# Optimization experiments

Hardware: AMD Instinct MI355X
Metric: run time of the kernel (lower is better)

The kernel has to match this reference:

```python
import jax, jax.numpy as jnp
import numpy as np

B, T, D = 8, 1024, 1024
H, G = 16, 4            # num_heads, query_groups
HD = D // H             # head_dim = 64
REP = H // G            # heads_per_group
EPS = 1e-10
NEG = -1e9


def setup_inputs() -> dict:
    key = jax.random.key(0)
    k1, k2, k3 = jax.random.split(key, 3)
    x = jax.random.normal(k1, (B, T, D), dtype=jnp.float32)
    w_qkv = jax.random.normal(k2, (D, H * HD + 2 * G * HD), dtype=jnp.float32) * (D ** -0.5)
    w_o = jax.random.normal(k3, (D, D), dtype=jnp.float32) * (D ** -0.5)
    padding_mask = jnp.ones((B, T), dtype=bool)
    return {"x": x, "w_qkv": w_qkv, "w_o": w_o, "padding_mask": padding_mask}


def _l2_norm(t):
    # qk_norm_type=2: L2 normalize over head_dim
    return t / (jnp.sqrt(jnp.sum(t * t, axis=-1, keepdims=True)) + EPS)


def reference(x, w_qkv, w_o, padding_mask):
    # fused QKV projection: [B,T,D] @ [D, H*HD + 2*G*HD]
    qkv = x @ w_qkv
    q, k, v = jnp.split(qkv, [H * HD, H * HD + G * HD], axis=-1)
    q = q.reshape(B, T, H, HD)
    k = k.reshape(B, T, G, HD)
    v = v.reshape(B, T, G, HD)
    # QK normalization (L2 over head_dim)
    q = _l2_norm(q)
    k = _l2_norm(k)
    # GQA: expand KV heads (repeat_interleave along head dim)
    k = jnp.repeat(k, REP, axis=2)  # [B,T,H,HD]
    v = jnp.repeat(v, REP, axis=2)
    # to [B,H,T,HD]
    q = q.transpose(0, 2, 1, 3)
    k = k.transpose(0, 2, 1, 3)
    v = v.transpose(0, 2, 1, 3)
    # causal + padding mask, True = attend
    causal = jnp.tril(jnp.ones((T, T), dtype=bool))  # [T_q, T_k]
    valid = padding_mask[:, None, :, None] & padding_mask[:, None, None, :] & causal[None, None]
    scale = HD ** -0.5  # SDPA default scale
    scores = jnp.einsum('bhqd,bhkd->bhqk', q, k) * scale
    scores = jnp.where(valid, scores, NEG)
    attn = jax.nn.softmax(scores, axis=-1)
    out = jnp.einsum('bhqk,bhkd->bhqd', attn, v)  # [B,H,T,HD]
    out = out.transpose(0, 2, 1, 3).reshape(B, T, D)
    return out @ w_o
```

## Files before the change

### kernel.cpp

```cpp
#include <hip/hip_runtime.h>
#include <hip/hip_bf16.h>

typedef __attribute__((ext_vector_type(8))) short short8;
typedef __attribute__((ext_vector_type(4))) short short4v;
typedef __attribute__((ext_vector_type(4))) float f32x4;

#define B_ 8
#define T_ 1024
#define D_ 1024
#define H_ 16
#define G_ 4
#define HD_ 64
#define QKVW 1536

#define GLOAD16(gp, lp) __builtin_amdgcn_global_load_lds( \
    (const __attribute__((address_space(1))) void*)(gp),  \
    (__attribute__((address_space(3))) void*)(lp), 16, 0, 0)

__device__ __forceinline__ float exp2_fast(float x) {
    return __builtin_amdgcn_exp2f(x);
}

__device__ __forceinline__ short8 pack_bf16x8(float4 a, float4 b) {
    union { short8 s; __hip_bfloat16 h[8]; } u;
    u.h[0] = __float2bfloat16(a.x); u.h[1] = __float2bfloat16(a.y);
    u.h[2] = __float2bfloat16(a.z); u.h[3] = __float2bfloat16(a.w);
    u.h[4] = __float2bfloat16(b.x); u.h[5] = __float2bfloat16(b.y);
    u.h[6] = __float2bfloat16(b.z); u.h[7] = __float2bfloat16(b.w);
    return u.s;
}

__global__ __launch_bounds__(256) void cvt_transpose(
    const float* __restrict__ in, __hip_bfloat16* __restrict__ outT, int K, int N)
{
    __shared__ float tile[32][33];
    const int k0 = blockIdx.y * 32, n0 = blockIdx.x * 32;
    const int r = threadIdx.x >> 5, c = threadIdx.x & 31;
    #pragma unroll
    for (int i = 0; i < 4; ++i)
        tile[r + i * 8][c] = in[(size_t)(k0 + r + i * 8) * N + n0 + c];
    __syncthreads();
    #pragma unroll
    for (int i = 0; i < 4; ++i)
        outT[(size_t)(n0 + r + i * 8) * K + k0 + c] = __float2bfloat16(tile[c][r + i * 8]);
}

__global__ __launch_bounds__(256) void gemm_qkv(
    const float* __restrict__ Af,
    const __hip_bfloat16* __restrict__ Bt,
    __hip_bfloat16* __restrict__ qkv,
    __hip_bfloat16* __restrict__ vt)
{
    const int M = B_ * T_, K = D_;
    __shared__ __hip_bfloat16 As[2][128 * 32];
    __shared__ __hip_bfloat16 Bs[2][128 * 32];

    const int tid  = threadIdx.x;
    const int lane = tid & 63;
    const int wr   = (tid >> 6) >> 1;
    const int wc   = (tid >> 6) & 1;

    const int rpx = (M >> 7) >> 3;
    const int xcd = blockIdx.x & 7;
    const int lin = blockIdx.x >> 3;
    const int by  = xcd * rpx + (lin % rpx);
    const int bx  = lin / rpx;
    const int m0 = by * 128;
    const int n0 = bx * 128;

    f32x4 acc[4][4] = {};

    const int sr0 = tid >> 2;
    const int sr1 = 64 + sr0;
    const int slot  = (tid & 3) ^ ((tid >> 3) & 3);
    const int sc_ln = (tid & 3) * 8;
    const int sc_sw = slot * 8;
    const int ws0 = sr0 * 64 + slot * 16;
    const int ws1 = sr1 * 64 + slot * 16;

    const float* Ar0f = Af + (size_t)(m0 + sr0) * K + sc_ln;
    const float* Ar1f = Af + (size_t)(m0 + sr1) * K + sc_ln;
    const __hip_bfloat16* Br0 = Bt + (size_t)(n0 + sr0) * K + sc_sw;
    const __hip_bfloat16* Br1 = Bt + (size_t)(n0 + sr1) * K + sc_sw;

    const int fr = lane & 15;
    const int kb = (lane >> 4) * 16;
    const int swzg = ((fr >> 1) & 3) << 4;

    float4 a0a = *(const float4*)(Ar0f);
    float4 a0b = *(const float4*)(Ar0f + 4);
    float4 a1a = *(const float4*)(Ar1f);
    float4 a1b = *(const float4*)(Ar1f + 4);
    GLOAD16(Br0, (char*)&Bs[0][0] + tid * 16);
    GLOAD16(Br1, (char*)&Bs[0][0] + 4096 + tid * 16);
    *(short8*)((char*)&As[0][0] + ws0) = pack_bf16x8(a0a, a0b);
    *(short8*)((char*)&As[0][0] + ws1) = pack_bf16x8(a1a, a1b);
    __syncthreads();

    int cur = 0;
    for (int kk = 0; kk < K; kk += 32) {
        const int nxt = cur ^ 1;
        const bool more = (kk + 32 < K);
        if (more) {
            a0a = *(const float4*)(Ar0f + kk + 32);
            a0b = *(const float4*)(Ar0f + kk + 36);
            a1a = *(const float4*)(Ar1f + kk + 32);
            a1b = *(const float4*)(Ar1f + kk + 36);
            GLOAD16(Br0 + kk + 32, (char*)&Bs[nxt][0] + tid * 16);
            GLOAD16(Br1 + kk + 32, (char*)&Bs[nxt][0] + 4096 + tid * 16);
        }
        short8 a[4], b[4];
        #pragma unroll
        for (int m = 0; m < 4; ++m)
            a[m] = *(const short8*)((char*)&As[cur][0] +
                    (wr * 64 + m * 16 + fr) * 64 + (kb ^ swzg));
        #pragma unroll
        for (int n = 0; n < 4; ++n)
            b[n] = *(const short8*)((char*)&Bs[cur][0] +
                    (wc * 64 + n * 16 + fr) * 64 + (kb ^ swzg));
        #pragma unroll
        for (int m = 0; m < 4; ++m)
            #pragma unroll
            for (int n = 0; n < 4; ++n)
                acc[m][n] = __builtin_amdgcn_mfma_f32_16x16x32_bf16(a[m], b[n], acc[m][n], 0, 0, 0);
        if (more) {
            *(short8*)((char*)&As[nxt][0] + ws0) = pack_bf16x8(a0a, a0b);
            *(short8*)((char*)&As[nxt][0] + ws1) = pack_bf16x8(a1a, a1b);
        }
        __syncthreads();
        cur = nxt;
    }

    const int rowb  = m0 + wr * 64 + (lane >> 4) * 4;
    const int colb0 = n0 + wc * 64;

    if (n0 < 1280) {
        const float extra = (n0 < 1024) ? 0.18033688f : 1.0f;
        #pragma unroll
        for (int m = 0; m < 4; ++m)
            #pragma unroll
            for (int r = 0; r < 4; ++r) {
                float ss = 0.f;
                #pragma unroll
                for (int n = 0; n < 4; ++n) { float v = acc[m][n][r]; ss += v * v; }
                ss += __shfl_xor(ss, 1, 64);
                ss += __shfl_xor(ss, 2, 64);
                ss += __shfl_xor(ss, 4, 64);
                ss += __shfl_xor(ss, 8, 64);
                float sc = extra / (sqrtf(ss) + 1e-10f);
                const size_t rbase = (size_t)(rowb + m * 16 + r) * QKVW + colb0 + fr;
                #pragma unroll
                for (int n = 0; n < 4; ++n)
                    qkv[rbase + n * 16] = __float2bfloat16(acc[m][n][r] * sc);
            }
    } else {
        #pragma unroll
        for (int m = 0; m < 4; ++m) {
            const int row = rowb + m * 16;
            const int bb  = row >> 10;
            const int t0  = row & 1023;
            #pragma unroll
            for (int n = 0; n < 4; ++n) {
                const int cv = colb0 + fr + n * 16 - 1280;
                const int gg = cv >> 6, d = cv & 63;
                union { short4v s; __hip_bfloat16 h[4]; } u;
                u.h[0] = __float2bfloat16(acc[m][n][0]);
                u.h[1] = __float2bfloat16(acc[m][n][1]);
                u.h[2] = __float2bfloat16(acc[m][n][2]);
                u.h[3] = __float2bfloat16(acc[m][n][3]);
                *reinterpret_cast<short4v*>(
                    vt + ((size_t)((bb * G_ + gg) * HD_ + d)) * T_ + t0) = u.s;
            }
        }
    }
}

__global__ __launch_bounds__(256) void gemm_tn_f32(
    const __hip_bfloat16* __restrict__ A,
    const __hip_bfloat16* __restrict__ Bt,
    float* __restrict__ C, int M, int N, int K)
{
    __shared__ __hip_bfloat16 As[2][128 * 32];
    __shared__ __hip_bfloat16 Bs[2][128 * 32];

    const int tid  = threadIdx.x;
    const int lane = tid & 63;
    const int wr   = (tid >> 6) >> 1;
    const int wc   = (tid >> 6) & 1;

    const int rpx = (M >> 7) >> 3;
    const int xcd = blockIdx.x & 7;
    const int lin = blockIdx.x >> 3;
    const int by  = xcd * rpx + (lin % rpx);
    const int bx  = lin / rpx;
    const int m0 = by * 128;
    const int n0 = bx * 128;

    f32x4 acc[4][4] = {};

    const int sr0 = tid >> 2;
    const int sr1 = 64 + sr0;
    const int slot  = (tid & 3) ^ ((tid >> 3) & 3);
    const int sc_sw = slot * 8;

    const __hip_bfloat16* Ar0 = A  + (size_t)(m0 + sr0) * K + sc_sw;
    const __hip_bfloat16* Ar1 = A  + (size_t)(m0 + sr1) * K + sc_sw;
    const __hip_bfloat16* Br0 = Bt + (size_t)(n0 + sr0) * K + sc_sw;
    const __hip_bfloat16* Br1 = Bt + (size_t)(n0 + sr1) * K + sc_sw;

    const int fr = lane & 15;
    const int kb = (lane >> 4) * 16;
    const int swzg = ((fr >> 1) & 3) << 4;

    GLOAD16(Ar0, (char*)&As[0][0] + tid * 16);
    GLOAD16(Ar1, (char*)&As[0][0] + 4096 + tid * 16);
    GLOAD16(Br0, (char*)&Bs[0][0] + tid * 16);
    GLOAD16(Br1, (char*)&Bs[0][0] + 4096 + tid * 16);
    __syncthreads();

    int cur = 0;
    for (int kk = 0; kk < K; kk += 32) {
        const int nxt = cur ^ 1;
        if (kk + 32 < K) {
            GLOAD16(Ar0 + kk + 32, (char*)&As[nxt][0] + tid * 16);
            GLOAD16(Ar1 + kk + 32, (char*)&As[nxt][0] + 4096 + tid * 16);
            GLOAD16(Br0 + kk + 32, (char*)&Bs[nxt][0] + tid * 16);
            GLOAD16(Br1 + kk + 32, (char*)&Bs[nxt][0] + 4096 + tid * 16);
        }
        short8 a[4], b[4];
        #pragma unroll
        for (int m = 0; m < 4; ++m)
            a[m] = *(const short8*)((char*)&As[cur][0] +
                    (wr * 64 + m * 16 + fr) * 64 + (kb ^ swzg));
        #pragma unroll
        for (int n = 0; n < 4; ++n)
            b[n] = *(const short8*)((char*)&Bs[cur][0] +
                    (wc * 64 + n * 16 + fr) * 64 + (kb ^ swzg));
        #pragma unroll
        for (int m = 0; m < 4; ++m)
            #pragma unroll
            for (int n = 0; n < 4; ++n)
                acc[m][n] = __builtin_amdgcn_mfma_f32_16x16x32_bf16(a[m], b[n], acc[m][n], 0, 0, 0);
        __syncthreads();
        cur = nxt;
    }

    const int rowb = m0 + wr * 64 + (lane >> 4) * 4;
    const int colb = n0 + wc * 64 + fr;
    #pragma unroll
    for (int m = 0; m < 4; ++m)
        #pragma unroll
        for (int n = 0; n < 4; ++n)
            #pragma unroll
            for (int r = 0; r < 4; ++r)
                C[(size_t)(rowb + m * 16 + r) * N + colb + n * 16] = acc[m][n][r];
}

__global__ __launch_bounds__(256) void attn_fwd(
    const __hip_bfloat16* __restrict__ qkv,
    const __hip_bfloat16* __restrict__ vt,
    __hip_bfloat16* __restrict__ out)
{
    const int pair = blockIdx.x;
    const int h  = blockIdx.y;
    const int b  = blockIdx.z;
    const int g  = h >> 2;

    const int tid  = threadIdx.x;
    const int lane = tid & 63;
    const int wid  = tid >> 6;

    __shared__ __hip_bfloat16 Ks[2 * 4096];
    __shared__ __hip_bfloat16 Vs[2 * 4096];
    __shared__ __hip_bfloat16 Ps[4 * 1024];

    const int fr  = lane & 15;
    const int kf  = (lane >> 4) * 8;
    const int kb  = kf * 2;
    const int swz = (fr & 7) << 4;

    const int srow = tid >> 3;
    const int scol = ((tid & 7) * 8) ^ ((srow & 7) << 3);

    const size_t kgbase = (size_t)(b * T_) * QKVW + H_ * HD_ + g * HD_ + scol;
    const size_t vgbase = (size_t)((b * G_ + g) * HD_) * T_ + scol;

    char* PsB = (char*)Ps + wid * 2048;

    auto stage = [&](int kt, int sl) {
        GLOAD16(qkv + kgbase + (size_t)(kt * 64 + srow) * QKVW,
                (char*)Ks + sl * 8192 + tid * 16);
        GLOAD16(qkv + kgbase + (size_t)(kt * 64 + 32 + srow) * QKVW,
                (char*)Ks + sl * 8192 + 4096 + tid * 16);
        GLOAD16(vt + vgbase + (size_t)srow * T_ + kt * 64,
                (char*)Vs + sl * 8192 + tid * 16);
        GLOAD16(vt + vgbase + (size_t)(32 + srow) * T_ + kt * 64,
                (char*)Vs + sl * 8192 + 4096 + tid * 16);
    };

    for (int half = 0; half < 2; ++half) {
        const int qt = half ? (15 - pair) : pair;
        const int q0 = qt * 64;
        const int arow  = q0 + wid * 16 + fr;
        const int rbase = q0 + wid * 16 + (lane >> 4) * 4;

        short8 qfrag0, qfrag1;
        {
            const size_t qbase = ((size_t)(b * T_ + arow)) * QKVW + h * HD_;
            qfrag0 = *(const short8*)(qkv + qbase + kf);
            qfrag1 = *(const short8*)(qkv + qbase + 32 + kf);
        }

        float lsum[4] = {0.f, 0.f, 0.f, 0.f};
        f32x4 o[4] = {};

        auto compute = [&](int kt, int sl, bool diag) {
            char* KsB = (char*)Ks + sl * 8192;
            char* VsB = (char*)Vs + sl * 8192;

            f32x4 s[4] = {};
            __builtin_amdgcn_s_setprio(1);
            #pragma unroll
            for (int nf = 0; nf < 4; ++nf) {
                const int row = fr + 16 * nf;
                short8 b0 = *(const short8*)(KsB + row * 128 + (kb ^ swz));
                short8 b1 = *(const short8*)(KsB + row * 128 + ((64 + kb) ^ swz));
                s[nf] = __builtin_amdgcn_mfma_f32_16x16x32_bf16(qfrag0, b0, s[nf], 0, 0, 0);
                s[nf] = __builtin_amdgcn_mfma_f32_16x16x32_bf16(qfrag1, b1, s[nf], 0, 0, 0);
            }
            __builtin_amdgcn_s_setprio(0);

            if (diag) {
                #pragma unroll
                for (int nf = 0; nf < 4; ++nf) {
                    int col = kt * 64 + fr + 16 * nf;
                    #pragma unroll
                    for (int r = 0; r < 4; ++r) {
                        float p = (col <= rbase + r) ? exp2_fast(s[nf][r]) : 0.f;
                        lsum[r] += p;
                        int q = (lane >> 4) * 4 + r;
                        *(__hip_bfloat16*)(PsB + q * 128 +
                            ((2 * (fr + 16 * nf)) ^ ((q & 7) << 4))) = __float2bfloat16(p);
                    }
                }
            } else {
                #pragma unroll
                for (int nf = 0; nf < 4; ++nf)
                    #pragma unroll
                    for (int r = 0; r < 4; ++r) {
                        float p = exp2_fast(s[nf][r]);
                        lsum[r] += p;
                        int q = (lane >> 4) * 4 + r;
                        *(__hip_bfloat16*)(PsB + q * 128 +
                            ((2 * (fr + 16 * nf)) ^ ((q & 7) << 4))) = __float2bfloat16(p);
                    }
            }

            short8 pa0 = *(const short8*)(PsB + fr * 128 + (kb ^ swz));
            short8 pa1 = *(const short8*)(PsB + fr * 128 + ((64 + kb) ^ swz));
            __builtin_amdgcn_s_setprio(1);
            #pragma unroll
            for (int nf = 0; nf < 4; ++nf) {
                const int row = fr + 16 * nf;
                short8 b0 = *(const short8*)(VsB + row * 128 + (kb ^ swz));
                short8 b1 = *(const short8*)(VsB + row * 128 + ((64 + kb) ^ swz));
                o[nf] = __builtin_amdgcn_mfma_f32_16x16x32_bf16(pa0, b0, o[nf], 0, 0, 0);
                o[nf] = __builtin_amdgcn_mfma_f32_16x16x32_bf16(pa1, b1, o[nf], 0, 0, 0);
            }
            __builtin_amdgcn_s_setprio(0);
        };

        int kt = 0;
        while (kt + 1 < qt) {
            stage(kt, 0);
            stage(kt + 1, 1);
            __syncthreads();
            compute(kt, 0, false);
            compute(kt + 1, 1, false);
            __syncthreads();
            kt += 2;
        }
        if (kt < qt) {
            stage(kt, 0);
            __syncthreads();
            compute(kt, 0, false);
            __syncthreads();
            kt += 1;
        }
        stage(qt, 0);
        __syncthreads();
        compute(qt, 0, true);
        __syncthreads();

        float linv[4];
        #pragma unroll
        for (int r = 0; r < 4; ++r) {
            float v = lsum[r];
            v += __shfl_xor(v, 1, 64);
            v += __shfl_xor(v, 2, 64);
            v += __shfl_xor(v, 4, 64);
            v += __shfl_xor(v, 8, 64);
            linv[r] = 1.0f / v;
        }
        #pragma unroll
        for (int nf = 0; nf < 4; ++nf) {
            int col = fr + 16 * nf;
            #pragma unroll
            for (int r = 0; r < 4; ++r) {
                float v = o[nf][r] * linv[r];
                out[((size_t)(b * T_ + rbase + r)) * (H_ * HD_) + h * HD_ + col] =
                    __float2bfloat16(v);
            }
        }
    }
}

extern "C" void kernel_launch(void* const* d_in, const int* in_sizes, int n_in,
                              void* d_out, int out_size, void* d_ws, size_t ws_size,
                              hipStream_t stream) {
    const float* x_f     = (const float*)d_in[0];
    const float* w_qkv_f = (const float*)d_in[1];
    const float* w_o_f   = (const float*)d_in[2];
    float* out = (float*)d_out;

    const int NX  = B_ * T_ * D_;
    const int NWQ = D_ * QKVW;
    const int NWO = D_ * D_;

    __hip_bfloat16* attn_out = (__hip_bfloat16*)d_ws;
    __hip_bfloat16* wqkvT = attn_out + NX;
    __hip_bfloat16* woT   = wqkvT + NWQ;
    __hip_bfloat16* qkv   = woT + NWO;
    __hip_bfloat16* vt    = qkv + (size_t)(B_ * T_) * QKVW;

    dim3 blk(256);

    cvt_transpose<<<dim3(QKVW / 32, D_ / 32), blk, 0, stream>>>(w_qkv_f, wqkvT, D_, QKVW);
    cvt_transpose<<<dim3(D_ / 32, D_ / 32), blk, 0, stream>>>(w_o_f, woT, D_, D_);

    gemm_qkv<<<dim3((QKVW / 128) * ((B_ * T_) / 128)), blk, 0, stream>>>(
        x_f, wqkvT, qkv, vt);

    attn_fwd<<<dim3(8, H_, B_), blk, 0, stream>>>(qkv, vt, attn_out);

    gemm_tn_f32<<<dim3((D_ / 128) * ((B_ * T_) / 128)), blk, 0, stream>>>(
        attn_out, woT, out, B_ * T_, D_, D_);
}
```

Before: 118.1 us.

## Enlarge attention query tile to 128 rows, two M-fragments per wave

The attention kernel now processes 128 query rows per block instead of 64, with each wave handling two 16-row fragments that share the K and V fragments loaded from LDS. This halves the number of blocks and the global K/V staging per query row, and reuses each LDS read of K/V for twice the MFMA work. It costs more registers and P scratch space and launches fewer blocks (512), which may hurt occupancy and load balance; the causal mask now covers the last two key tiles.

```diff
diff --git a/kernel.cpp b/kernel.cpp
--- a/kernel.cpp
+++ b/kernel.cpp
@@ -272,7 +272,7 @@
 
     __shared__ __hip_bfloat16 Ks[2 * 4096];
     __shared__ __hip_bfloat16 Vs[2 * 4096];
-    __shared__ __hip_bfloat16 Ps[4 * 1024];
+    __shared__ __hip_bfloat16 Ps[4 * 2048];
 
     const int fr  = lane & 15;
     const int kf  = (lane >> 4) * 8;
@@ -285,7 +285,7 @@
     const size_t kgbase = (size_t)(b * T_) * QKVW + H_ * HD_ + g * HD_ + scol;
     const size_t vgbase = (size_t)((b * G_ + g) * HD_) * T_ + scol;
 
-    char* PsB = (char*)Ps + wid * 2048;
+    char* PsB = (char*)Ps + wid * 4096;
 
     auto stage = [&](int kt, int sl) {
         GLOAD16(qkv + kgbase + (size_t)(kt * 64 + srow) * QKVW,
@@ -299,117 +299,125 @@
     };
 
     for (int half = 0; half < 2; ++half) {
-        const int qt = half ? (15 - pair) : pair;
-        const int q0 = qt * 64;
-        const int arow  = q0 + wid * 16 + fr;
-        const int rbase = q0 + wid * 16 + (lane >> 4) * 4;
-
-        short8 qfrag0, qfrag1;
-        {
-            const size_t qbase = ((size_t)(b * T_ + arow)) * QKVW + h * HD_;
-            qfrag0 = *(const short8*)(qkv + qbase + kf);
-            qfrag1 = *(const short8*)(qkv + qbase + 32 + kf);
-        }
-
-        float lsum[4] = {0.f, 0.f, 0.f, 0.f};
-        f32x4 o[4] = {};
-
-        auto compute = [&](int kt, int sl, bool diag) {
-            char* KsB = (char*)Ks + sl * 8192;
-            char* VsB = (char*)Vs + sl * 8192;
-
-            f32x4 s[4] = {};
-            __builtin_amdgcn_s_setprio(1);
-            #pragma unroll
-            for (int nf = 0; nf < 4; ++nf) {
-                const int row = fr + 16 * nf;
-                short8 b0 = *(const short8*)(KsB + row * 128 + (kb ^ swz));
-                short8 b1 = *(const short8*)(KsB + row * 128 + ((64 + kb) ^ swz));
-                s[nf] = __builtin_amdgcn_mfma_f32_16x16x32_bf16(qfrag0, b0, s[nf], 0, 0, 0);
-                s[nf] = __builtin_amdgcn_mfma_f32_16x16x32_bf16(qfrag1, b1, s[nf], 0, 0, 0);
-            }
-            __builtin_amdgcn_s_setprio(0);
-
-            if (diag) {
-                #pragma unroll
-                for (int nf = 0; nf < 4; ++nf) {
-                    int col = kt * 64 + fr + 16 * nf;
-                    #pragma unroll
-                    for (int r = 0; r < 4; ++r) {
-                        float p = (col <= rbase + r) ? exp2_fast(s[nf][r]) : 0.f;
-                        lsum[r] += p;
-                        int q = (lane >> 4) * 4 + r;
-                        *(__hip_bfloat16*)(PsB + q * 128 +
-                            ((2 * (fr + 16 * nf)) ^ ((q & 7) << 4))) = __float2bfloat16(p);
-                    }
-                }
-            } else {
-                #pragma unroll
-                for (int nf = 0; nf < 4; ++nf)
-                    #pragma unroll
-                    for (int r = 0; r < 4; ++r) {
-                        float p = exp2_fast(s[nf][r]);
-                        lsum[r] += p;
-                        int q = (lane >> 4) * 4 + r;
-                        *(__hip_bfloat16*)(PsB + q * 128 +
-                            ((2 * (fr + 16 * nf)) ^ ((q & 7) << 4))) = __float2bfloat16(p);
-                    }
-            }
-
-            short8 pa0 = *(const short8*)(PsB + fr * 128 + (kb ^ swz));
-            short8 pa1 = *(const short8*)(PsB + fr * 128 + ((64 + kb) ^ swz));
-            __builtin_amdgcn_s_setprio(1);
-            #pragma unroll
-            for (int nf = 0; nf < 4; ++nf) {
-                const int row = fr + 16 * nf;
-                short8 b0 = *(const short8*)(VsB + row * 128 + (kb ^ swz));
-                short8 b1 = *(const short8*)(VsB + row * 128 + ((64 + kb) ^ swz));
-                o[nf] = __builtin_amdgcn_mfma_f32_16x16x32_bf16(pa0, b0, o[nf], 0, 0, 0);
-                o[nf] = __builtin_amdgcn_mfma_f32_16x16x32_bf16(pa1, b1, o[nf], 0, 0, 0);
-            }
-            __builtin_amdgcn_s_setprio(0);
-        };
-
-        int kt = 0;
-        while (kt + 1 < qt) {
+        const int qt  = half ? (7 - pair) : pair;
+        const int q0  = qt * 128;
+        const int nkt = 2 * qt + 2;
+
+        short8 qf[2][2];
+        #pragma unroll
+        for (int m = 0; m < 2; ++m) {
+            const size_t qbase =
+                ((size_t)(b * T_ + q0 + wid * 32 + m * 16 + fr)) * QKVW + h * HD_;
+            qf[m][0] = *(const short8*)(qkv + qbase + kf);
+            qf[m][1] = *(const short8*)(qkv + qbase + 32 + kf);
+        }
+        const int rb0 = q0 + wid * 32 + (lane >> 4) * 4;
+
+        float lsum[2][4] = {};
+        f32x4 o[2][4] = {};
+
+        for (int kt = 0; kt < nkt; kt += 2) {
             stage(kt, 0);
             stage(kt + 1, 1);
             __syncthreads();
-            compute(kt, 0, false);
-            compute(kt + 1, 1, false);
+
+            #pragma unroll
+            for (int sl = 0; sl < 2; ++sl) {
+                const int  ck  = kt + sl;
+                const bool msk = (ck >= nkt - 2);
+                char* KsB = (char*)Ks + sl * 8192;
+                char* VsB = (char*)Vs + sl * 8192;
+
+                short8 bk0[4], bk1[4];
+                #pragma unroll
+                for (int nf = 0; nf < 4; ++nf) {
+                    const int row = fr + 16 * nf;
+                    bk0[nf] = *(const short8*)(KsB + row * 128 + (kb ^ swz));
+                    bk1[nf] = *(const short8*)(KsB + row * 128 + ((64 + kb) ^ swz));
+                }
+
+                #pragma unroll
+                for (int m = 0; m < 2; ++m) {
+                    f32x4 s[4] = {};
+                    __builtin_amdgcn_s_setprio(1);
+                    #pragma unroll
+                    for (int nf = 0; nf < 4; ++nf) {
+                        s[nf] = __builtin_amdgcn_mfma_f32_16x16x32_bf16(qf[m][0], bk0[nf], s[nf], 0, 0, 0);
+                        s[nf] = __builtin_amdgcn_mfma_f32_16x16x32_bf16(qf[m][1], bk1[nf], s[nf], 0, 0, 0);
+                    }
+                    __builtin_amdgcn_s_setprio(0);
+
+                    if (msk) {
+                        #pragma unroll
+                        for (int nf = 0; nf < 4; ++nf) {
+                            int col = ck * 64 + fr + 16 * nf;
+                            #pragma unroll
+                            for (int r = 0; r < 4; ++r) {
+                                float p = (col <= rb0 + m * 16 + r) ? exp2_fast(s[nf][r]) : 0.f;
+                                lsum[m][r] += p;
+                                int q = m * 16 + (lane >> 4) * 4 + r;
+                                *(__hip_bfloat16*)(PsB + q * 128 +
+                                    ((2 * (fr + 16 * nf)) ^ ((q & 7) << 4))) = __float2bfloat16(p);
+                            }
+                        }
+                    } else {
+                        #pragma unroll
+                        for (int nf = 0; nf < 4; ++nf)
+                            #pragma unroll
+                            for (int r = 0; r < 4; ++r) {
+                                float p = exp2_fast(s[nf][r]);
+                                lsum[m][r] += p;
+                                int q = m * 16 + (lane >> 4) * 4 + r;
+                                *(__hip_bfloat16*)(PsB + q * 128 +
+                                    ((2 * (fr + 16 * nf)) ^ ((q & 7) << 4))) = __float2bfloat16(p);
+                            }
+                    }
+                }
+
+                short8 bv0[4], bv1[4];
+                #pragma unroll
+                for (int nf = 0; nf < 4; ++nf) {
+                    const int row = fr + 16 * nf;
+                    bv0[nf] = *(const short8*)(VsB + row * 128 + (kb ^ swz));
+                    bv1[nf] = *(const short8*)(VsB + row * 128 + ((64 + kb) ^ swz));
+                }
+                __builtin_amdgcn_s_setprio(1);
+                #pragma unroll
+                for (int m = 0; m < 2; ++m) {
+                    short8 pa0 = *(const short8*)(PsB + (m * 16 + fr) * 128 + (kb ^ swz));
+                    short8 pa1 = *(const short8*)(PsB + (m * 16 + fr) * 128 + ((64 + kb) ^ swz));
+                    #pragma unroll
+                    for (int nf = 0; nf < 4; ++nf) {
+                        o[m][nf] = __builtin_amdgcn_mfma_f32_16x16x32_bf16(pa0, bv0[nf], o[m][nf], 0, 0, 0);
+                        o[m][nf] = __builtin_amdgcn_mfma_f32_16x16x32_bf16(pa1, bv1[nf], o[m][nf], 0, 0, 0);
+                    }
+                }
+                __builtin_amdgcn_s_setprio(0);
+            }
             __syncthreads();
-            kt += 2;
-        }
-        if (kt < qt) {
-            stage(kt, 0);
-            __syncthreads();
-            compute(kt, 0, false);
-            __syncthreads();
-            kt += 1;
-        }
-        stage(qt, 0);
-        __syncthreads();
-        compute(qt, 0, true);
-        __syncthreads();
-
-        float linv[4];
-        #pragma unroll
-        for (int r = 0; r < 4; ++r) {
-            float v = lsum[r];
-            v += __shfl_xor(v, 1, 64);
-            v += __shfl_xor(v, 2, 64);
-            v += __shfl_xor(v, 4, 64);
-            v += __shfl_xor(v, 8, 64);
-            linv[r] = 1.0f / v;
-        }
-        #pragma unroll
-        for (int nf = 0; nf < 4; ++nf) {
-            int col = fr + 16 * nf;
+        }
+
+        #pragma unroll
+        for (int m = 0; m < 2; ++m) {
+            float linv[4];
             #pragma unroll
             for (int r = 0; r < 4; ++r) {
-                float v = o[nf][r] * linv[r];
-                out[((size_t)(b * T_ + rbase + r)) * (H_ * HD_) + h * HD_ + col] =
-                    __float2bfloat16(v);
+                float v = lsum[m][r];
+                v += __shfl_xor(v, 1, 64);
+                v += __shfl_xor(v, 2, 64);
+                v += __shfl_xor(v, 4, 64);
+                v += __shfl_xor(v, 8, 64);
+                linv[r] = 1.0f / v;
+            }
+            #pragma unroll
+            for (int nf = 0; nf < 4; ++nf) {
+                int col = fr + 16 * nf;
+                #pragma unroll
+                for (int r = 0; r < 4; ++r) {
+                    float v = o[m][nf][r] * linv[r];
+                    out[((size_t)(b * T_ + rb0 + m * 16 + r)) * (H_ * HD_) + h * HD_ + col] =
+                        __float2bfloat16(v);
+                }
             }
         }
     }
@@ -441,7 +449,7 @@
     gemm_qkv<<<dim3((QKVW / 128) * ((B_ * T_) / 128)), blk, 0, stream>>>(
         x_f, wqkvT, qkv, vt);
 
-    attn_fwd<<<dim3(8, H_, B_), blk, 0, stream>>>(qkv, vt, attn_out);
+    attn_fwd<<<dim3(4, H_, B_), blk, 0, stream>>>(qkv, vt, attn_out);
 
     gemm_tn_f32<<<dim3((D_ / 128) * ((B_ * T_) / 128)), blk, 0, stream>>>(
         attn_out, woT, out, B_ * T_, D_, D_);
```

After: 115.0 us. 2.6% less time.
